# Kernel tuning notes

Measured on AMD Instinct MI355X. Metric: run time of the kernel, lower is better.

Reference implementation:

```python
import jax, jax.numpy as jnp
import numpy as np

N = 50000      # nodes
E = 800000     # directed edges
D = 128        # input_dim == hidden_dim
EL = 100000    # edges scored by decoder


def setup_inputs() -> dict:
    key = jax.random.key(0)
    ks = jax.random.split(key, 8)
    s = 1.0 / np.sqrt(D)  # glorot-ish scale
    return {
        "node_feature": jax.random.normal(ks[0], (N, D), jnp.float32),
        "W1": jax.random.normal(ks[1], (D, D), jnp.float32) * s,
        "b1": jnp.zeros((D,), jnp.float32),
        "W2": jax.random.normal(ks[2], (D, D), jnp.float32) * s,
        "b2": jnp.zeros((D,), jnp.float32),
        "W3": jax.random.normal(ks[3], (D, D), jnp.float32) * s,
        "b3": jnp.zeros((D,), jnp.float32),
        "edge_index": jax.random.randint(ks[4], (2, E), 0, N, dtype=jnp.int32),
        "edge_label_index": jax.random.randint(ks[5], (2, EL), 0, N, dtype=jnp.int32),
    }


def _gcn_conv(x, W, b, src, dst, norm, n):
    # x' = D^{-1/2} (A + I) D^{-1/2} (x W) + b   (PyG GCNConv semantics)
    h = x @ W                                   # [N, D]
    msg = h[src] * norm[:, None]                # gather + scale, [E+N, D]
    out = jax.ops.segment_sum(msg, dst, num_segments=n)  # scatter-add
    return out + b


def reference(node_feature, W1, b1, W2, b2, W3, b3, edge_index, edge_label_index):
    n = node_feature.shape[0]
    loop = jnp.arange(n, dtype=edge_index.dtype)
    src = jnp.concatenate([edge_index[0], loop])  # self-loops appended
    dst = jnp.concatenate([edge_index[1], loop])
    # symmetric normalization: deg over destinations (incl. self-loops)
    deg = jax.ops.segment_sum(jnp.ones_like(dst, dtype=node_feature.dtype), dst, num_segments=n)
    dinv = jax.lax.rsqrt(jnp.maximum(deg, 1.0))
    norm = dinv[src] * dinv[dst]                 # [E+N]

    x = jax.nn.relu(_gcn_conv(node_feature, W1, b1, src, dst, norm, n))
    x = jax.nn.relu(_gcn_conv(x, W2, b2, src, dst, norm, n))
    x = _gcn_conv(x, W3, b3, src, dst, norm, n)

    # dot-product edge decoder
    u = x[edge_label_index[0]]
    v = x[edge_label_index[1]]
    return jnp.sum(u * v, axis=-1)               # [EL] logits
```

## Files before the change

### kernel.cpp

```cpp
#include <hip/hip_runtime.h>
#include <hip/hip_bf16.h>
#include <hip/hip_fp16.h>

typedef _Float16 v8h __attribute__((ext_vector_type(8)));
typedef float v4f __attribute__((ext_vector_type(4)));

__global__ __launch_bounds__(256) void gemm1_deg(const float* __restrict__ X,
                                                 const float* __restrict__ W,
                                                 __half* __restrict__ H, int Nrows,
                                                 int gemmBlocks, int degBlocks,
                                                 const int* __restrict__ dst,
                                                 int* __restrict__ cnt,
                                                 int* __restrict__ rank, int E,
                                                 const float* __restrict__ W2,
                                                 const float* __restrict__ W3,
                                                 __half* __restrict__ wfrag) {
    int tid = threadIdx.x;
    if (blockIdx.x >= gemmBlocks + degBlocks) {
        int o = (blockIdx.x - gemmBlocks - degBlocks) * 256 + tid;
        int w = o >> 14, r = o & 16383;
        const float* Ws = w ? W3 : W2;
        int k = r >> 7, ncol = r & 127;
        int c = ncol >> 4, nl = ncol & 15;
        int s = k >> 5, quad = (k >> 3) & 3, j = k & 7;
        int di = ((c * 4 + s) * 64 + quad * 16 + nl) * 8 + j;
        wfrag[(size_t)w * 16384 + di] = __float2half_rn(Ws[r]);
        return;
    }
    if (blockIdx.x >= gemmBlocks) {
        int base = (blockIdx.x - gemmBlocks) * 1024 + tid * 4;
        if (base + 3 < E) {
            int d0 = dst[base], d1 = dst[base + 1], d2 = dst[base + 2], d3 = dst[base + 3];
            int r0 = atomicAdd(&cnt[d0], 1);
            int r1 = atomicAdd(&cnt[d1], 1);
            int r2 = atomicAdd(&cnt[d2], 1);
            int r3 = atomicAdd(&cnt[d3], 1);
            rank[base] = r0; rank[base + 1] = r1; rank[base + 2] = r2; rank[base + 3] = r3;
        } else {
            for (int e = base; e < E; ++e) rank[e] = atomicAdd(&cnt[dst[e]], 1);
        }
        return;
    }
    __shared__ __align__(16) float xs[16][132];
    __shared__ __align__(16) float ws[16][128];
    int tx = tid & 15;
    int ty = tid >> 4;
    int row0 = blockIdx.x * 128;
    float acc[8][8] = {};
    for (int k0 = 0; k0 < 128; k0 += 16) {
        {
            int r = tid >> 2;
            int j = (tid & 3) * 4;
            int gr = row0 + r;
            float4 v = (gr < Nrows) ? *(const float4*)&X[(size_t)gr * 128 + k0 + j]
                                    : make_float4(0.f, 0.f, 0.f, 0.f);
            xs[j + 0][r] = v.x; xs[j + 1][r] = v.y; xs[j + 2][r] = v.z; xs[j + 3][r] = v.w;
            int gr2 = gr + 64;
            float4 u = (gr2 < Nrows) ? *(const float4*)&X[(size_t)gr2 * 128 + k0 + j]
                                     : make_float4(0.f, 0.f, 0.f, 0.f);
            xs[j + 0][r + 64] = u.x; xs[j + 1][r + 64] = u.y;
            xs[j + 2][r + 64] = u.z; xs[j + 3][r + 64] = u.w;
        }
        {
            const float4* Wv = (const float4*)&W[(size_t)k0 * 128];
            float4* wsv = (float4*)&ws[0][0];
            wsv[tid] = Wv[tid];
            wsv[tid + 256] = Wv[tid + 256];
        }
        __syncthreads();
#pragma unroll
        for (int kk = 0; kk < 16; ++kk) {
            float4 xa = *(float4*)&xs[kk][ty * 4];
            float4 xb = *(float4*)&xs[kk][ty * 4 + 64];
            float4 wa = *(float4*)&ws[kk][tx * 4];
            float4 wb = *(float4*)&ws[kk][tx * 4 + 64];
            float xr[8] = {xa.x, xa.y, xa.z, xa.w, xb.x, xb.y, xb.z, xb.w};
            float wr[8] = {wa.x, wa.y, wa.z, wa.w, wb.x, wb.y, wb.z, wb.w};
#pragma unroll
            for (int i = 0; i < 8; ++i)
#pragma unroll
                for (int j = 0; j < 8; ++j)
                    acc[i][j] += xr[i] * wr[j];
        }
        __syncthreads();
    }
    auto pk = [](float x, float y) { __half2 h = __floats2half2_rn(x, y); return *(unsigned int*)&h; };
#pragma unroll
    for (int i = 0; i < 8; ++i) {
        int gr = row0 + ((i < 4) ? (ty * 4 + i) : (64 + ty * 4 + i - 4));
        if (gr < Nrows) {
            uint2 q0 = make_uint2(pk(acc[i][0], acc[i][1]), pk(acc[i][2], acc[i][3]));
            uint2 q1 = make_uint2(pk(acc[i][4], acc[i][5]), pk(acc[i][6], acc[i][7]));
            *(uint2*)&H[(size_t)gr * 128 + tx * 4] = q0;
            *(uint2*)&H[(size_t)gr * 128 + 64 + tx * 4] = q1;
        }
    }
}

__global__ __launch_bounds__(256) void agg_gemm(const __half* __restrict__ Xs,
                                                const float* __restrict__ dinv,
                                                const int* __restrict__ rowptr,
                                                const int* __restrict__ col,
                                                const __half* __restrict__ wfrag,
                                                const float* __restrict__ bias,
                                                __half* __restrict__ Out,
                                                int n, int finalLayer) {
    __shared__ __align__(16) _Float16 y[64][136];
    int tid = threadIdx.x;
    int rowbase = blockIdx.x * 64;
    {
        int sub = tid >> 4;
        int t = (tid & 15) * 8;
        for (int g = 0; g < 4; ++g) {
            int rr = g * 16 + sub;
            int node = rowbase + rr;
            float a[8] = {};
            if (node < n) {
                int beg = rowptr[node], end = rowptr[node + 1];
                int k = beg;
                for (; k + 4 <= end; k += 4) {
                    int s0 = col[k], s1 = col[k + 1], s2 = col[k + 2], s3 = col[k + 3];
                    uint4 r0 = *(const uint4*)&Xs[(size_t)s0 * 128 + t];
                    uint4 r1 = *(const uint4*)&Xs[(size_t)s1 * 128 + t];
                    uint4 r2 = *(const uint4*)&Xs[(size_t)s2 * 128 + t];
                    uint4 r3 = *(const uint4*)&Xs[(size_t)s3 * 128 + t];
                    const __half2* h0 = (const __half2*)&r0;
                    const __half2* h1 = (const __half2*)&r1;
                    const __half2* h2 = (const __half2*)&r2;
                    const __half2* h3 = (const __half2*)&r3;
#pragma unroll
                    for (int m = 0; m < 4; ++m) {
                        float2 f0 = __half22float2(h0[m]);
                        float2 f1 = __half22float2(h1[m]);
                        float2 f2 = __half22float2(h2[m]);
                        float2 f3 = __half22float2(h3[m]);
                        a[2 * m]     += (f0.x + f1.x) + (f2.x + f3.x);
                        a[2 * m + 1] += (f0.y + f1.y) + (f2.y + f3.y);
                    }
                }
                for (; k < end; ++k) {
                    uint4 r0 = *(const uint4*)&Xs[(size_t)col[k] * 128 + t];
                    const __half2* h0 = (const __half2*)&r0;
#pragma unroll
                    for (int m = 0; m < 4; ++m) {
                        float2 f0 = __half22float2(h0[m]);
                        a[2 * m] += f0.x;
                        a[2 * m + 1] += f0.y;
                    }
                }
                float dn = dinv[node];
#pragma unroll
                for (int m = 0; m < 8; ++m) a[m] *= dn;
            }
            v8h yv;
#pragma unroll
            for (int m = 0; m < 8; ++m) yv[m] = (_Float16)a[m];
            *(v8h*)&y[rr][t] = yv;
        }
    }
    __syncthreads();
    int l = tid & 63;
    int wid = tid >> 6;
    int rb = wid * 16;
    int quad = l >> 4;
    int nn = l & 15;
    v8h a0 = *(const v8h*)&y[rb + nn][0 * 32 + quad * 8];
    v8h a1 = *(const v8h*)&y[rb + nn][1 * 32 + quad * 8];
    v8h a2 = *(const v8h*)&y[rb + nn][2 * 32 + quad * 8];
    v8h a3 = *(const v8h*)&y[rb + nn][3 * 32 + quad * 8];
    const v8h* Wf = (const v8h*)wfrag;
    v4f acc[8] = {};
#pragma unroll
    for (int c = 0; c < 8; ++c) {
        v8h b0 = Wf[(c * 4 + 0) * 64 + l];
        v8h b1 = Wf[(c * 4 + 1) * 64 + l];
        v8h b2 = Wf[(c * 4 + 2) * 64 + l];
        v8h b3 = Wf[(c * 4 + 3) * 64 + l];
        acc[c] = __builtin_amdgcn_mfma_f32_16x16x32_f16(a0, b0, acc[c], 0, 0, 0);
        acc[c] = __builtin_amdgcn_mfma_f32_16x16x32_f16(a1, b1, acc[c], 0, 0, 0);
        acc[c] = __builtin_amdgcn_mfma_f32_16x16x32_f16(a2, b2, acc[c], 0, 0, 0);
        acc[c] = __builtin_amdgcn_mfma_f32_16x16x32_f16(a3, b3, acc[c], 0, 0, 0);
    }
#pragma unroll
    for (int reg = 0; reg < 4; ++reg) {
        int gr = rowbase + rb + quad * 4 + reg;
        if (gr < n) {
            float dn = dinv[gr];
#pragma unroll
            for (int c = 0; c < 8; ++c) {
                float z = acc[c][reg] + bias[c * 16 + nn];
                if (!finalLayer) z = fmaxf(z, 0.f) * dn;
                Out[(size_t)gr * 128 + c * 16 + nn] = __float2half_rn(z);
            }
        }
    }
}

__global__ void scanA(const int* __restrict__ cnt, int* __restrict__ tmp,
                      int* __restrict__ bsum, int n) {
    __shared__ int s[256];
    int i = blockIdx.x * 256 + threadIdx.x;
    int v = (i < n) ? (cnt[i] + 1) : 0;
    s[threadIdx.x] = v;
    __syncthreads();
    for (int off = 1; off < 256; off <<= 1) {
        int x = (threadIdx.x >= off) ? s[threadIdx.x - off] : 0;
        __syncthreads();
        s[threadIdx.x] += x;
        __syncthreads();
    }
    if (i < n) tmp[i] = s[threadIdx.x];
    if (threadIdx.x == 255) bsum[blockIdx.x] = s[255];
}

__global__ void scanB(const int* __restrict__ tmp, const int* __restrict__ bsum,
                      const int* __restrict__ cnt, int* __restrict__ rowptr,
                      float* __restrict__ dinv, int* __restrict__ col, int n, int nb) {
    __shared__ int p[256];
    int t = threadIdx.x;
    p[t] = (t < nb) ? bsum[t] : 0;
    __syncthreads();
    for (int off = 1; off < 256; off <<= 1) {
        int x = (t >= off) ? p[t - off] : 0;
        __syncthreads();
        p[t] += x;
        __syncthreads();
    }
    int prefix = (blockIdx.x == 0) ? 0 : p[blockIdx.x - 1];
    int i = blockIdx.x * 256 + t;
    if (i < n) {
        int inc = tmp[i] + prefix;
        rowptr[i + 1] = inc;
        int c1 = cnt[i] + 1;
        dinv[i] = rsqrtf((float)c1);
        col[inc - c1] = i;
        if (i == 0) rowptr[0] = 0;
    }
}

__global__ __launch_bounds__(256) void fill4(const int* __restrict__ src,
                                             const int* __restrict__ dst,
                                             const int* __restrict__ rank,
                                             const int* __restrict__ rowptr,
                                             int* __restrict__ col, int E) {
    int base = blockIdx.x * 1024 + threadIdx.x * 4;
    if (base + 3 < E) {
        int d0 = dst[base], d1 = dst[base + 1], d2 = dst[base + 2], d3 = dst[base + 3];
        int s0 = src[base], s1 = src[base + 1], s2 = src[base + 2], s3 = src[base + 3];
        int r0 = rank[base], r1 = rank[base + 1], r2 = rank[base + 2], r3 = rank[base + 3];
        col[rowptr[d0] + 1 + r0] = s0;
        col[rowptr[d1] + 1 + r1] = s1;
        col[rowptr[d2] + 1 + r2] = s2;
        col[rowptr[d3] + 1 + r3] = s3;
    } else {
        for (int e = base; e < E; ++e)
            col[rowptr[dst[e]] + 1 + rank[e]] = src[e];
    }
}

__global__ __launch_bounds__(256) void agg_h(const __half* __restrict__ H,
                                             const float* __restrict__ dinv,
                                             const int* __restrict__ rowptr,
                                             const int* __restrict__ col,
                                             const float* __restrict__ bias,
                                             __half* __restrict__ out, int n) {
    int node = blockIdx.x * 16 + (threadIdx.x >> 4);
    int t = (threadIdx.x & 15) * 8;
    if (node >= n) return;
    int beg = rowptr[node], end = rowptr[node + 1];
    float a[8] = {};
    int k = beg;
    for (; k + 4 <= end; k += 4) {
        int s0 = col[k], s1 = col[k + 1], s2 = col[k + 2], s3 = col[k + 3];
        float w0 = dinv[s0], w1 = dinv[s1], w2 = dinv[s2], w3 = dinv[s3];
        uint4 r0 = *(const uint4*)&H[(size_t)s0 * 128 + t];
        uint4 r1 = *(const uint4*)&H[(size_t)s1 * 128 + t];
        uint4 r2 = *(const uint4*)&H[(size_t)s2 * 128 + t];
        uint4 r3 = *(const uint4*)&H[(size_t)s3 * 128 + t];
        const __half2* h0 = (const __half2*)&r0;
        const __half2* h1 = (const __half2*)&r1;
        const __half2* h2 = (const __half2*)&r2;
        const __half2* h3 = (const __half2*)&r3;
#pragma unroll
        for (int m = 0; m < 4; ++m) {
            float2 f0 = __half22float2(h0[m]);
            float2 f1 = __half22float2(h1[m]);
            float2 f2 = __half22float2(h2[m]);
            float2 f3 = __half22float2(h3[m]);
            a[2 * m]     += f0.x * w0 + f1.x * w1 + f2.x * w2 + f3.x * w3;
            a[2 * m + 1] += f0.y * w0 + f1.y * w1 + f2.y * w2 + f3.y * w3;
        }
    }
    for (; k < end; ++k) {
        int s0 = col[k];
        float w0 = dinv[s0];
        uint4 r0 = *(const uint4*)&H[(size_t)s0 * 128 + t];
        const __half2* h0 = (const __half2*)&r0;
#pragma unroll
        for (int m = 0; m < 4; ++m) {
            float2 f0 = __half22float2(h0[m]);
            a[2 * m] += f0.x * w0;
            a[2 * m + 1] += f0.y * w0;
        }
    }
    float dn = dinv[node];
    float4 b0 = *(const float4*)&bias[t];
    float4 b1 = *(const float4*)&bias[t + 4];
    float r0 = fmaxf(a[0] * dn + b0.x, 0.f) * dn;
    float r1 = fmaxf(a[1] * dn + b0.y, 0.f) * dn;
    float r2 = fmaxf(a[2] * dn + b0.z, 0.f) * dn;
    float r3 = fmaxf(a[3] * dn + b0.w, 0.f) * dn;
    float r4 = fmaxf(a[4] * dn + b1.x, 0.f) * dn;
    float r5 = fmaxf(a[5] * dn + b1.y, 0.f) * dn;
    float r6 = fmaxf(a[6] * dn + b1.z, 0.f) * dn;
    float r7 = fmaxf(a[7] * dn + b1.w, 0.f) * dn;
    auto pk = [](float x, float y) { __half2 h = __floats2half2_rn(x, y); return *(unsigned int*)&h; };
    uint4 o = make_uint4(pk(r0, r1), pk(r2, r3), pk(r4, r5), pk(r6, r7));
    *(uint4*)&out[(size_t)node * 128 + t] = o;
}

__global__ __launch_bounds__(256) void decoder_h(const __half* __restrict__ X,
                                                 const int* __restrict__ eli,
                                                 float* __restrict__ out, int EL) {
    int e = blockIdx.x * 16 + (threadIdx.x >> 4);
    int lane = threadIdx.x & 15;
    if (e >= EL) return;
    int u = eli[e], v = eli[EL + e];
    uint4 ra = *(const uint4*)&X[(size_t)u * 128 + lane * 8];
    uint4 rb = *(const uint4*)&X[(size_t)v * 128 + lane * 8];
    const __half2* ha = (const __half2*)&ra;
    const __half2* hb = (const __half2*)&rb;
    float d = 0.f;
#pragma unroll
    for (int j = 0; j < 4; ++j) {
        float2 fa = __half22float2(ha[j]);
        float2 fb = __half22float2(hb[j]);
        d += fa.x * fb.x + fa.y * fb.y;
    }
#pragma unroll
    for (int off = 8; off > 0; off >>= 1) d += __shfl_xor(d, off);
    if (lane == 0) out[e] = d;
}

extern "C" void kernel_launch(void* const* d_in, const int* in_sizes, int n_in,
                              void* d_out, int out_size, void* d_ws, size_t ws_size,
                              hipStream_t stream) {
    const float* x0 = (const float*)d_in[0];
    const float* W1 = (const float*)d_in[1];
    const float* b1 = (const float*)d_in[2];
    const float* W2 = (const float*)d_in[3];
    const float* b2 = (const float*)d_in[4];
    const float* W3 = (const float*)d_in[5];
    const float* b3 = (const float*)d_in[6];
    const int* ei   = (const int*)d_in[7];
    const int* eli  = (const int*)d_in[8];
    float* out = (float*)d_out;

    const int D = 128;
    const int N  = in_sizes[0] / D;
    const int E  = in_sizes[7] / 2;
    const int EL = in_sizes[8] / 2;

    const int* src = ei;
    const int* dst = ei + E;

    char* ws = (char*)d_ws;
    size_t off = 0;
    auto alloc = [&](size_t bytes) -> void* {
        off = (off + 255) & ~(size_t)255;
        void* p = ws + off;
        off += bytes;
        return p;
    };
    int*    cnt    = (int*)alloc((size_t)N * sizeof(int));
    int*    tmp    = (int*)alloc((size_t)N * sizeof(int));
    int*    bsum   = (int*)alloc(256 * sizeof(int));
    int*    rowptr = (int*)alloc((size_t)(N + 1) * sizeof(int));
    float*  dinv   = (float*)alloc((size_t)N * sizeof(float));
    int*    rank   = (int*)alloc((size_t)E * sizeof(int));
    int*    col    = (int*)alloc((size_t)(E + N) * sizeof(int));
    __half* wfrag  = (__half*)alloc((size_t)2 * 16384 * sizeof(__half));
    __half* hbuf   = (__half*)alloc((size_t)N * D * sizeof(__half));
    __half* xbuf   = (__half*)alloc((size_t)N * D * sizeof(__half));
    (void)ws_size;

    hipMemsetAsync(cnt, 0, (size_t)N * sizeof(int), stream);

    int nbN = (N + 255) / 256;
    int nbE4 = (E + 1023) / 1024;
    int gemmGrid = (N + 127) / 128;
    int fusedGrid = (N + 63) / 64;
    int aggGrid  = (N + 15) / 16;

    gemm1_deg<<<gemmGrid + nbE4 + 128, 256, 0, stream>>>(x0, W1, hbuf, N,
                                                         gemmGrid, nbE4,
                                                         dst, cnt, rank, E,
                                                         W2, W3, wfrag);

    scanA<<<nbN, 256, 0, stream>>>(cnt, tmp, bsum, N);
    scanB<<<nbN, 256, 0, stream>>>(tmp, bsum, cnt, rowptr, dinv, col, N, nbN);
    fill4<<<nbE4, 256, 0, stream>>>(src, dst, rank, rowptr, col, E);

    agg_h<<<aggGrid, 256, 0, stream>>>(hbuf, dinv, rowptr, col, b1, xbuf, N);
    agg_gemm<<<fusedGrid, 256, 0, stream>>>(xbuf, dinv, rowptr, col, wfrag, b2, hbuf, N, 0);
    agg_gemm<<<fusedGrid, 256, 0, stream>>>(hbuf, dinv, rowptr, col, wfrag + 16384, b3, xbuf, N, 1);

    decoder_h<<<(EL + 15) / 16, 256, 0, stream>>>(xbuf, eli, out, EL);
}
```

Measured before the change: 273.1 us.

## Run first-layer GEMM on MFMA with split-fp16 precision compensation

Replaces the scalar fp32 layer-1 GEMM with fp16 MFMA instructions. Input rows and W1 are each split into high and low fp16 parts, and three MFMA products are accumulated in fp32 to approximate fp32 accuracy. Weight swizzling moves into its own kernel launch that also produces the W1 hi/lo fragments. This trades extra MFMA work and an additional launch for much faster matrix math on a first layer that reads fp32 input. The output stores are per-element fp16 writes that are strided rather than vectorized.

```diff
diff --git a/kernel.cpp b/kernel.cpp
--- a/kernel.cpp
+++ b/kernel.cpp
@@ -3,30 +3,39 @@
 #include <hip/hip_fp16.h>
 
 typedef _Float16 v8h __attribute__((ext_vector_type(8)));
+typedef _Float16 v4h __attribute__((ext_vector_type(4)));
 typedef float v4f __attribute__((ext_vector_type(4)));
 
-__global__ __launch_bounds__(256) void gemm1_deg(const float* __restrict__ X,
-                                                 const float* __restrict__ W,
-                                                 __half* __restrict__ H, int Nrows,
-                                                 int gemmBlocks, int degBlocks,
-                                                 const int* __restrict__ dst,
-                                                 int* __restrict__ cnt,
-                                                 int* __restrict__ rank, int E,
-                                                 const float* __restrict__ W2,
-                                                 const float* __restrict__ W3,
-                                                 __half* __restrict__ wfrag) {
+__global__ __launch_bounds__(256) void wswz(const float* __restrict__ W1,
+                                            const float* __restrict__ W2,
+                                            const float* __restrict__ W3,
+                                            __half* __restrict__ wfrag) {
+    int o = blockIdx.x * 256 + threadIdx.x;
+    int w = o >> 14, r = o & 16383;
+    const float* Ws = (w >= 3) ? W3 : ((w == 2) ? W2 : W1);
+    float v = Ws[r];
+    __half h;
+    if (w == 1) {
+        __half hv = __float2half_rn(v);
+        h = __float2half_rn(v - __half2float(hv));
+    } else {
+        h = __float2half_rn(v);
+    }
+    int k = r >> 7, ncol = r & 127;
+    int c = ncol >> 4, nl = ncol & 15;
+    int s = k >> 5, quad = (k >> 3) & 3, j = k & 7;
+    int di = ((c * 4 + s) * 64 + quad * 16 + nl) * 8 + j;
+    wfrag[(size_t)w * 16384 + di] = h;
+}
+
+__global__ __launch_bounds__(256) void gemm1_mfma(const float* __restrict__ X,
+                                                  const __half* __restrict__ wfrag,
+                                                  __half* __restrict__ H, int Nrows,
+                                                  int gemmBlocks,
+                                                  const int* __restrict__ dst,
+                                                  int* __restrict__ cnt,
+                                                  int* __restrict__ rank, int E) {
     int tid = threadIdx.x;
-    if (blockIdx.x >= gemmBlocks + degBlocks) {
-        int o = (blockIdx.x - gemmBlocks - degBlocks) * 256 + tid;
-        int w = o >> 14, r = o & 16383;
-        const float* Ws = w ? W3 : W2;
-        int k = r >> 7, ncol = r & 127;
-        int c = ncol >> 4, nl = ncol & 15;
-        int s = k >> 5, quad = (k >> 3) & 3, j = k & 7;
-        int di = ((c * 4 + s) * 64 + quad * 16 + nl) * 8 + j;
-        wfrag[(size_t)w * 16384 + di] = __float2half_rn(Ws[r]);
-        return;
-    }
     if (blockIdx.x >= gemmBlocks) {
         int base = (blockIdx.x - gemmBlocks) * 1024 + tid * 4;
         if (base + 3 < E) {
@@ -41,58 +50,75 @@
         }
         return;
     }
-    __shared__ __align__(16) float xs[16][132];
-    __shared__ __align__(16) float ws[16][128];
-    int tx = tid & 15;
-    int ty = tid >> 4;
-    int row0 = blockIdx.x * 128;
-    float acc[8][8] = {};
-    for (int k0 = 0; k0 < 128; k0 += 16) {
-        {
-            int r = tid >> 2;
-            int j = (tid & 3) * 4;
-            int gr = row0 + r;
-            float4 v = (gr < Nrows) ? *(const float4*)&X[(size_t)gr * 128 + k0 + j]
-                                    : make_float4(0.f, 0.f, 0.f, 0.f);
-            xs[j + 0][r] = v.x; xs[j + 1][r] = v.y; xs[j + 2][r] = v.z; xs[j + 3][r] = v.w;
-            int gr2 = gr + 64;
-            float4 u = (gr2 < Nrows) ? *(const float4*)&X[(size_t)gr2 * 128 + k0 + j]
-                                     : make_float4(0.f, 0.f, 0.f, 0.f);
-            xs[j + 0][r + 64] = u.x; xs[j + 1][r + 64] = u.y;
-            xs[j + 2][r + 64] = u.z; xs[j + 3][r + 64] = u.w;
-        }
-        {
-            const float4* Wv = (const float4*)&W[(size_t)k0 * 128];
-            float4* wsv = (float4*)&ws[0][0];
-            wsv[tid] = Wv[tid];
-            wsv[tid + 256] = Wv[tid + 256];
-        }
-        __syncthreads();
-#pragma unroll
-        for (int kk = 0; kk < 16; ++kk) {
-            float4 xa = *(float4*)&xs[kk][ty * 4];
-            float4 xb = *(float4*)&xs[kk][ty * 4 + 64];
-            float4 wa = *(float4*)&ws[kk][tx * 4];
-            float4 wb = *(float4*)&ws[kk][tx * 4 + 64];
-            float xr[8] = {xa.x, xa.y, xa.z, xa.w, xb.x, xb.y, xb.z, xb.w};
-            float wr[8] = {wa.x, wa.y, wa.z, wa.w, wb.x, wb.y, wb.z, wb.w};
-#pragma unroll
-            for (int i = 0; i < 8; ++i)
-#pragma unroll
-                for (int j = 0; j < 8; ++j)
-                    acc[i][j] += xr[i] * wr[j];
-        }
-        __syncthreads();
-    }
-    auto pk = [](float x, float y) { __half2 h = __floats2half2_rn(x, y); return *(unsigned int*)&h; };
-#pragma unroll
-    for (int i = 0; i < 8; ++i) {
-        int gr = row0 + ((i < 4) ? (ty * 4 + i) : (64 + ty * 4 + i - 4));
+    __shared__ __align__(16) _Float16 xh[64][136];
+    __shared__ __align__(16) _Float16 xl[64][136];
+    int rowbase = blockIdx.x * 64;
+#pragma unroll
+    for (int it = 0; it < 8; ++it) {
+        int idx = it * 256 + tid;
+        int row = idx >> 5;
+        int cq = idx & 31;
+        int gr = rowbase + row;
+        float4 v = (gr < Nrows) ? *(const float4*)&X[(size_t)gr * 128 + cq * 4]
+                                : make_float4(0.f, 0.f, 0.f, 0.f);
+        float f[4] = {v.x, v.y, v.z, v.w};
+        v4h hv, lv;
+#pragma unroll
+        for (int m = 0; m < 4; ++m) {
+            _Float16 h = (_Float16)f[m];
+            hv[m] = h;
+            lv[m] = (_Float16)(f[m] - (float)h);
+        }
+        *(v4h*)&xh[row][cq * 4] = hv;
+        *(v4h*)&xl[row][cq * 4] = lv;
+    }
+    __syncthreads();
+    int l = tid & 63;
+    int wid = tid >> 6;
+    int rb = wid * 16;
+    int quad = l >> 4;
+    int nn = l & 15;
+    v8h ah0 = *(const v8h*)&xh[rb + nn][0 * 32 + quad * 8];
+    v8h ah1 = *(const v8h*)&xh[rb + nn][1 * 32 + quad * 8];
+    v8h ah2 = *(const v8h*)&xh[rb + nn][2 * 32 + quad * 8];
+    v8h ah3 = *(const v8h*)&xh[rb + nn][3 * 32 + quad * 8];
+    v8h al0 = *(const v8h*)&xl[rb + nn][0 * 32 + quad * 8];
+    v8h al1 = *(const v8h*)&xl[rb + nn][1 * 32 + quad * 8];
+    v8h al2 = *(const v8h*)&xl[rb + nn][2 * 32 + quad * 8];
+    v8h al3 = *(const v8h*)&xl[rb + nn][3 * 32 + quad * 8];
+    const v8h* Wh = (const v8h*)wfrag;
+    const v8h* Wl = (const v8h*)(wfrag + 16384);
+    v4f acc[8] = {};
+#pragma unroll
+    for (int c = 0; c < 8; ++c) {
+        v8h bh0 = Wh[(c * 4 + 0) * 64 + l];
+        v8h bh1 = Wh[(c * 4 + 1) * 64 + l];
+        v8h bh2 = Wh[(c * 4 + 2) * 64 + l];
+        v8h bh3 = Wh[(c * 4 + 3) * 64 + l];
+        acc[c] = __builtin_amdgcn_mfma_f32_16x16x32_f16(ah0, bh0, acc[c], 0, 0, 0);
+        acc[c] = __builtin_amdgcn_mfma_f32_16x16x32_f16(ah1, bh1, acc[c], 0, 0, 0);
+        acc[c] = __builtin_amdgcn_mfma_f32_16x16x32_f16(ah2, bh2, acc[c], 0, 0, 0);
+        acc[c] = __builtin_amdgcn_mfma_f32_16x16x32_f16(ah3, bh3, acc[c], 0, 0, 0);
+        acc[c] = __builtin_amdgcn_mfma_f32_16x16x32_f16(al0, bh0, acc[c], 0, 0, 0);
+        acc[c] = __builtin_amdgcn_mfma_f32_16x16x32_f16(al1, bh1, acc[c], 0, 0, 0);
+        acc[c] = __builtin_amdgcn_mfma_f32_16x16x32_f16(al2, bh2, acc[c], 0, 0, 0);
+        acc[c] = __builtin_amdgcn_mfma_f32_16x16x32_f16(al3, bh3, acc[c], 0, 0, 0);
+        v8h bl0 = Wl[(c * 4 + 0) * 64 + l];
+        v8h bl1 = Wl[(c * 4 + 1) * 64 + l];
+        v8h bl2 = Wl[(c * 4 + 2) * 64 + l];
+        v8h bl3 = Wl[(c * 4 + 3) * 64 + l];
+        acc[c] = __builtin_amdgcn_mfma_f32_16x16x32_f16(ah0, bl0, acc[c], 0, 0, 0);
+        acc[c] = __builtin_amdgcn_mfma_f32_16x16x32_f16(ah1, bl1, acc[c], 0, 0, 0);
+        acc[c] = __builtin_amdgcn_mfma_f32_16x16x32_f16(ah2, bl2, acc[c], 0, 0, 0);
+        acc[c] = __builtin_amdgcn_mfma_f32_16x16x32_f16(ah3, bl3, acc[c], 0, 0, 0);
+    }
+#pragma unroll
+    for (int reg = 0; reg < 4; ++reg) {
+        int gr = rowbase + rb + quad * 4 + reg;
         if (gr < Nrows) {
-            uint2 q0 = make_uint2(pk(acc[i][0], acc[i][1]), pk(acc[i][2], acc[i][3]));
-            uint2 q1 = make_uint2(pk(acc[i][4], acc[i][5]), pk(acc[i][6], acc[i][7]));
-            *(uint2*)&H[(size_t)gr * 128 + tx * 4] = q0;
-            *(uint2*)&H[(size_t)gr * 128 + 64 + tx * 4] = q1;
+#pragma unroll
+            for (int c = 0; c < 8; ++c)
+                H[(size_t)gr * 128 + c * 16 + nn] = __float2half_rn(acc[c][reg]);
         }
     }
 }
@@ -379,7 +405,7 @@
     float*  dinv   = (float*)alloc((size_t)N * sizeof(float));
     int*    rank   = (int*)alloc((size_t)E * sizeof(int));
     int*    col    = (int*)alloc((size_t)(E + N) * sizeof(int));
-    __half* wfrag  = (__half*)alloc((size_t)2 * 16384 * sizeof(__half));
+    __half* wfrag  = (__half*)alloc((size_t)4 * 16384 * sizeof(__half));
     __half* hbuf   = (__half*)alloc((size_t)N * D * sizeof(__half));
     __half* xbuf   = (__half*)alloc((size_t)N * D * sizeof(__half));
     (void)ws_size;
@@ -388,22 +414,22 @@
 
     int nbN = (N + 255) / 256;
     int nbE4 = (E + 1023) / 1024;
-    int gemmGrid = (N + 127) / 128;
+    int gemmGrid = (N + 63) / 64;
     int fusedGrid = (N + 63) / 64;
     int aggGrid  = (N + 15) / 16;
 
-    gemm1_deg<<<gemmGrid + nbE4 + 128, 256, 0, stream>>>(x0, W1, hbuf, N,
-                                                         gemmGrid, nbE4,
-                                                         dst, cnt, rank, E,
-                                                         W2, W3, wfrag);
+    wswz<<<256, 256, 0, stream>>>(W1, W2, W3, wfrag);
+
+    gemm1_mfma<<<gemmGrid + nbE4, 256, 0, stream>>>(x0, wfrag, hbuf, N,
+                                                    gemmGrid, dst, cnt, rank, E);
 
     scanA<<<nbN, 256, 0, stream>>>(cnt, tmp, bsum, N);
     scanB<<<nbN, 256, 0, stream>>>(tmp, bsum, cnt, rowptr, dinv, col, N, nbN);
     fill4<<<nbE4, 256, 0, stream>>>(src, dst, rank, rowptr, col, E);
 
     agg_h<<<aggGrid, 256, 0, stream>>>(hbuf, dinv, rowptr, col, b1, xbuf, N);
-    agg_gemm<<<fusedGrid, 256, 0, stream>>>(xbuf, dinv, rowptr, col, wfrag, b2, hbuf, N, 0);
-    agg_gemm<<<fusedGrid, 256, 0, stream>>>(hbuf, dinv, rowptr, col, wfrag + 16384, b3, xbuf, N, 1);
+    agg_gemm<<<fusedGrid, 256, 0, stream>>>(xbuf, dinv, rowptr, col, wfrag + 2 * 16384, b2, hbuf, N, 0);
+    agg_gemm<<<fusedGrid, 256, 0, stream>>>(hbuf, dinv, rowptr, col, wfrag + 3 * 16384, b3, xbuf, N, 1);
 
     decoder_h<<<(EL + 15) / 16, 256, 0, stream>>>(xbuf, eli, out, EL);
 }
```

After: 265.0 us. 3.0% less time.
